# Optimization experiments

Hardware: AMD Instinct MI355X
Metric: run time of the kernel (lower is better)

The kernel has to match this reference:

```python
import jax, jax.numpy as jnp
import numpy as np

B, S, T, E, H, F = 2, 2048, 2048, 1024, 16, 4096
HD = E // H
EPS = 1e-5


def setup_inputs() -> dict:
    key = jax.random.key(0)
    ks = jax.random.split(key, 16)
    def w(k, shape):
        return (jax.random.normal(k, shape, jnp.float32) * 0.02)
    d = {
        "x": jax.random.normal(ks[0], (B, S, E), jnp.float32),
        "enc": jax.random.normal(ks[1], (B, T, E), jnp.float32),
    }
    for i, n in enumerate(["sa_q", "sa_k", "sa_v", "sa_o", "ca_q", "ca_k", "ca_v", "ca_o"]):
        d[n + "w"] = w(ks[2 + i], (E, E))  # torch Linear: [out, in]
        d[n + "b"] = jnp.zeros((E,), jnp.float32)
    d["w1"] = w(ks[10], (F, E)); d["b1"] = jnp.zeros((F,), jnp.float32)
    d["w2"] = w(ks[11], (E, F)); d["b2"] = jnp.zeros((E,), jnp.float32)
    for n in ["ln1", "ln2", "ln3"]:
        d[n + "_g"] = jnp.ones((E,), jnp.float32)
        d[n + "_b"] = jnp.zeros((E,), jnp.float32)
    return d


def _layernorm(x, g, b):
    m = jnp.mean(x, axis=-1, keepdims=True)
    v = jnp.mean((x - m) ** 2, axis=-1, keepdims=True)
    return (x - m) / jnp.sqrt(v + EPS) * g + b


def _heads(x, w, b):
    bsz, sl, _ = x.shape
    y = x @ w.T + b
    return y.reshape(bsz, sl, H, HD).transpose(0, 2, 1, 3)  # [B,H,S,hd]


def _mha(xq, xkv, qw, qb, kw, kb, vw, vb, ow, ob, causal):
    q = _heads(xq, qw, qb)
    k = _heads(xkv, kw, kb)
    v = _heads(xkv, vw, vb)
    scores = jnp.einsum('bhsd,bhtd->bhst', q, k) / np.sqrt(HD).astype(np.float32)
    if causal:
        sl, tl = scores.shape[-2], scores.shape[-1]
        mask = jnp.tril(jnp.ones((sl, tl), bool))
        scores = jnp.where(mask, scores, -jnp.inf)
    a = jax.nn.softmax(scores, axis=-1)
    o = jnp.einsum('bhst,bhtd->bhsd', a, v)
    o = o.transpose(0, 2, 1, 3).reshape(xq.shape[0], xq.shape[1], E)
    return o @ ow.T + ob


def reference(x, enc,
              sa_qw, sa_qb, sa_kw, sa_kb, sa_vw, sa_vb, sa_ow, sa_ob,
              ca_qw, ca_qb, ca_kw, ca_kb, ca_vw, ca_vb, ca_ow, ca_ob,
              w1, b1, w2, b2,
              ln1_g, ln1_b, ln2_g, ln2_b, ln3_g, ln3_b):
    sa = _mha(x, x, sa_qw, sa_qb, sa_kw, sa_kb, sa_vw, sa_vb, sa_ow, sa_ob, True)
    x = _layernorm(x + sa, ln1_g, ln1_b)
    ca = _mha(x, enc, ca_qw, ca_qb, ca_kw, ca_kb, ca_vw, ca_vb, ca_ow, ca_ob, False)
    x = _layernorm(x + ca, ln2_g, ln2_b)
    ffn = jax.nn.relu(x @ w1.T + b1) @ w2.T + b2
    return _layernorm(x + ffn, ln3_g, ln3_b)
```

## Files before the change

kernel.cpp:

```cpp
#include <hip/hip_runtime.h>
#include <hip/hip_bf16.h>
#include <stdint.h>

typedef __attribute__((ext_vector_type(8))) short s16x8;
typedef __attribute__((ext_vector_type(4))) short s16x4;
typedef __attribute__((ext_vector_type(4))) float f32x4;

#define DEV static __device__ __forceinline__

DEV ushort f2bu(float f){
  unsigned u = __builtin_bit_cast(unsigned, f);
  return (ushort)((u + 0x7fffu + ((u >> 16) & 1u)) >> 16);
}
DEV ushort f2bn(float f){
  return __builtin_bit_cast(ushort, __float2bfloat16(f));
}

DEV void gload16(const void* g, void* l){
  __builtin_amdgcn_global_load_lds((const __attribute__((address_space(1))) void*)g,
                                   (__attribute__((address_space(3))) void*)l, 16, 0, 0);
}

struct ConvArgs {
  const float* src[17];
  void*        dst[17];
  int blk_end[17];
  int nel[17];
  unsigned f32mask;
};

__global__ void __launch_bounds__(256) k_conv(ConvArgs a){
  int bi = blockIdx.x, seg = 0;
  while (bi >= a.blk_end[seg]) seg++;
  int b0 = seg ? a.blk_end[seg-1] : 0;
  long off = (long)(bi - b0)*2048 + (long)threadIdx.x*8;
  if (off >= a.nel[seg]) return;
  const float* s = a.src[seg] + off;
  f32x4 v0 = *(const f32x4*)s;
  f32x4 v1 = *(const f32x4*)(s+4);
  if ((a.f32mask >> seg) & 1u){
    float* d = (float*)a.dst[seg] + off;
    *(f32x4*)d = v0; *(f32x4*)(d+4) = v1;
  } else {
    ushort* d = (ushort*)a.dst[seg] + off;
    s16x8 o;
#pragma unroll
    for (int j = 0; j < 4; j++){ o[j] = (short)f2bu(v0[j]); o[4+j] = (short)f2bu(v1[j]); }
    *(s16x8*)d = o;
  }
}

template<int MODE, bool DBUF>
__global__ void __launch_bounds__(256) k_gemm(const ushort* __restrict__ A, const ushort* __restrict__ W,
    const float* __restrict__ bias, float* __restrict__ Cf, ushort* __restrict__ Cb,
    int M, int N, int Kext, int lda, int ldb, long long sstride)
{
  constexpr int NB = DBUF ? 2 : 1;
  __shared__ __align__(16) ushort lsA[NB][128*64];
  __shared__ __align__(16) ushort lsB[NB][128*64];
  const int t = threadIdx.x, w = t >> 6, u = t & 63, lr = u & 15, lk = u >> 4;
  const int m0 = blockIdx.y * 128, n0 = blockIdx.x * 128;
  const int s = blockIdx.z;
  const int wm = w >> 1, wn = w & 1;
  const int rA = t >> 3, c8 = (t & 7) * 8;
  const ushort* Ap = A + (size_t)(m0 + rA) * lda + (size_t)s * Kext + c8;
  const ushort* Wp = W + (size_t)(n0 + rA) * ldb + (size_t)s * Kext + c8;
  if (s){ bias = nullptr; if (Cf) Cf += sstride; }
  f32x4 acc[4][4] = {};
  const int nk = Kext >> 6;

  auto stage = [&](int k0, int buf){
#pragma unroll
    for (int j = 0; j < 4; j++){
      gload16(Ap + (size_t)j*32*lda + k0, &lsA[buf][0] + j*2048 + w*512);
      gload16(Wp + (size_t)j*32*ldb + k0, &lsB[buf][0] + j*2048 + w*512);
    }
  };
  auto body = [&](const ushort* La, const ushort* Lb){
#pragma unroll
    for (int ks = 0; ks < 2; ks++){
      s16x8 af[4], bfr[4];
#pragma unroll
      for (int i = 0; i < 4; i++) af[i]  = *(const s16x8*)(La + (wm*64 + i*16 + lr)*64 + ks*32 + lk*8);
#pragma unroll
      for (int i = 0; i < 4; i++) bfr[i] = *(const s16x8*)(Lb + (wn*64 + i*16 + lr)*64 + ks*32 + lk*8);
#pragma unroll
      for (int mi = 0; mi < 4; mi++)
#pragma unroll
        for (int ni = 0; ni < 4; ni++)
          acc[mi][ni] = __builtin_amdgcn_mfma_f32_16x16x32_bf16(af[mi], bfr[ni], acc[mi][ni], 0, 0, 0);
    }
  };

  if (DBUF){
    stage(0, 0);
    for (int tk = 0; tk < nk; ++tk){
      __syncthreads();
      if (tk + 1 < nk) stage((tk + 1) << 6, (tk + 1) & 1);
      body(&lsA[tk & 1][0], &lsB[tk & 1][0]);
    }
  } else {
    for (int tk = 0; tk < nk; ++tk){
      stage(tk << 6, 0);
      __syncthreads();
      body(&lsA[0][0], &lsB[0][0]);
      __syncthreads();
    }
  }

#pragma unroll
  for (int mi = 0; mi < 4; mi++){
#pragma unroll
    for (int ni = 0; ni < 4; ni++){
      const int row = m0 + wm*64 + mi*16 + lk*4;
      const int col = n0 + wn*64 + ni*16 + lr;
      const float bv = bias ? bias[col] : 0.f;
#pragma unroll
      for (int i = 0; i < 4; i++){
        float v = acc[mi][ni][i] + bv;
        if (MODE == 2) v = fmaxf(v, 0.f);
        size_t idx = (size_t)(row + i) * N + col;
        if (MODE == 1) Cf[idx] = v; else Cb[idx] = f2bn(v);
      }
    }
  }
}

template<int MODE>
__global__ void __launch_bounds__(512, 1) k_gemm256(const ushort* __restrict__ A, const ushort* __restrict__ W,
    const float* __restrict__ bias, float* __restrict__ Cf, ushort* __restrict__ Cb,
    int N, int K, int lda, int ldb)
{
  __shared__ __align__(16) ushort lsA[2][256*64];
  __shared__ __align__(16) ushort lsB[2][256*64];
  const int t = threadIdx.x, w = t >> 6, u = t & 63, lr = u & 15, lk = u >> 4;
  const int gx = gridDim.x;
  const int nwg = gx * gridDim.y;
  const int id = blockIdx.y * gx + blockIdx.x;
  const int swz = (id & 7) * (nwg >> 3) + (id >> 3);
  const int n0 = (swz % gx) * 256, m0 = (swz / gx) * 256;
  const int wm = w >> 2, wn = w & 3;

  const int r0 = w*8 + (u >> 3), cc = u & 7;
  const int csw = 8 * (cc ^ (r0 & 7));
  const ushort* Ap = A + (size_t)(m0 + r0) * lda + csw;
  const ushort* Wp = W + (size_t)(n0 + r0) * ldb + csw;

  f32x4 acc[8][4] = {};
  const int nt = K >> 6;
  const int swl = lr & 7;
  s16x8 afr[4], bfr[4];

#pragma unroll
  for (int j = 0; j < 4; j++){
    gload16(Ap + (size_t)(64*j)*lda, &lsA[0][0] + w*512 + j*4096);
    gload16(Wp + (size_t)(64*j)*ldb, &lsB[0][0] + w*512 + j*4096);
  }
  asm volatile("s_waitcnt vmcnt(0)" ::: "memory");
  __builtin_amdgcn_s_barrier();

  for (int tk = 0; tk < nt; ++tk){
    const char* La = (const char*)&lsA[tk & 1][0];
    const char* Lb = (const char*)&lsB[tk & 1][0];
    ushort* dA = &lsA[(tk & 1) ^ 1][0] + w*512;
    ushort* dB = &lsB[(tk & 1) ^ 1][0] + w*512;
    const bool pf = (tk + 1 < nt);
    const size_t k1 = (size_t)(tk + 1) << 6;

#pragma unroll
    for (int i = 0; i < 4; i++)
      afr[i] = *(const s16x8*)(La + (wm*128 + i*16 + lr)*128 + ((lk ^ swl) * 16));
#pragma unroll
    for (int i = 0; i < 4; i++)
      bfr[i] = *(const s16x8*)(Lb + (wn*64 + i*16 + lr)*128 + ((lk ^ swl) * 16));
    if (pf){
      gload16(Ap + k1, dA);
      gload16(Wp + k1, dB);
      gload16(Ap + (size_t)64*lda + k1, dA + 4096);
      gload16(Wp + (size_t)64*ldb + k1, dB + 4096);
    }
    __builtin_amdgcn_s_barrier();
    asm volatile("s_waitcnt lgkmcnt(0)" ::: "memory");
    __builtin_amdgcn_s_setprio(1);
#pragma unroll
    for (int mi = 0; mi < 4; mi++)
#pragma unroll
      for (int ni = 0; ni < 4; ni++)
        acc[mi][ni] = __builtin_amdgcn_mfma_f32_16x16x32_bf16(afr[mi], bfr[ni], acc[mi][ni], 0, 0, 0);
    __builtin_amdgcn_s_setprio(0);
    __builtin_amdgcn_s_barrier();

#pragma unroll
    for (int i = 0; i < 4; i++)
      afr[i] = *(const s16x8*)(La + (wm*128 + 64 + i*16 + lr)*128 + ((lk ^ swl) * 16));
    if (pf){
      gload16(Ap + (size_t)128*lda + k1, dA + 8192);
      gload16(Wp + (size_t)128*ldb + k1, dB + 8192);
      gload16(Ap + (size_t)192*lda + k1, dA + 12288);
      gload16(Wp + (size_t)192*ldb + k1, dB + 12288);
    }
    __builtin_amdgcn_s_barrier();
    asm volatile("s_waitcnt lgkmcnt(0)" ::: "memory");
    __builtin_amdgcn_s_setprio(1);
#pragma unroll
    for (int mi = 0; mi < 4; mi++)
#pragma unroll
      for (int ni = 0; ni < 4; ni++)
        acc[4+mi][ni] = __builtin_amdgcn_mfma_f32_16x16x32_bf16(afr[mi], bfr[ni], acc[4+mi][ni], 0, 0, 0);
    __builtin_amdgcn_s_setprio(0);
    __builtin_amdgcn_s_barrier();

#pragma unroll
    for (int i = 0; i < 4; i++)
      afr[i] = *(const s16x8*)(La + (wm*128 + i*16 + lr)*128 + (((4 + lk) ^ swl) * 16));
#pragma unroll
    for (int i = 0; i < 4; i++)
      bfr[i] = *(const s16x8*)(Lb + (wn*64 + i*16 + lr)*128 + (((4 + lk) ^ swl) * 16));
    __builtin_amdgcn_s_barrier();
    asm volatile("s_waitcnt lgkmcnt(0)" ::: "memory");
    __builtin_amdgcn_s_setprio(1);
#pragma unroll
    for (int mi = 0; mi < 4; mi++)
#pragma unroll
      for (int ni = 0; ni < 4; ni++)
        acc[mi][ni] = __builtin_amdgcn_mfma_f32_16x16x32_bf16(afr[mi], bfr[ni], acc[mi][ni], 0, 0, 0);
    __builtin_amdgcn_s_setprio(0);
    __builtin_amdgcn_s_barrier();

#pragma unroll
    for (int i = 0; i < 4; i++)
      afr[i] = *(const s16x8*)(La + (wm*128 + 64 + i*16 + lr)*128 + (((4 + lk) ^ swl) * 16));
    __builtin_amdgcn_s_barrier();
    asm volatile("s_waitcnt lgkmcnt(0)" ::: "memory");
    __builtin_amdgcn_s_setprio(1);
#pragma unroll
    for (int mi = 0; mi < 4; mi++)
#pragma unroll
      for (int ni = 0; ni < 4; ni++)
        acc[4+mi][ni] = __builtin_amdgcn_mfma_f32_16x16x32_bf16(afr[mi], bfr[ni], acc[4+mi][ni], 0, 0, 0);
    __builtin_amdgcn_s_setprio(0);
    asm volatile("s_waitcnt vmcnt(0)" ::: "memory");
    __builtin_amdgcn_s_barrier();
  }

#pragma unroll
  for (int mi = 0; mi < 8; mi++){
#pragma unroll
    for (int ni = 0; ni < 4; ni++){
      const int row = m0 + wm*128 + mi*16 + lk*4;
      const int col = n0 + wn*64 + ni*16 + lr;
      const float bv = bias ? bias[col] : 0.f;
#pragma unroll
      for (int i = 0; i < 4; i++){
        float v = acc[mi][ni][i] + bv;
        if (MODE == 2) v = fmaxf(v, 0.f);
        size_t idx = (size_t)(row + i) * N + col;
        if (MODE == 1) Cf[idx] = v; else Cb[idx] = f2bn(v);
      }
    }
  }
}

__global__ void __launch_bounds__(256) k_vt(const ushort* __restrict__ V, ushort* __restrict__ Vt,
                                            int stride, int S)
{
  __shared__ ushort tile[64][72];
  const int st = blockIdx.x*64, h = blockIdx.y, b = blockIdx.z;
  const int r = threadIdx.x >> 3, c8 = (threadIdx.x & 7)*8;
#pragma unroll
  for (int j = 0; j < 2; j++){
    int s = r + j*32;
    s16x8 v = *(const s16x8*)(V + (size_t)(b*S + st + s)*stride + h*64 + c8);
    *(s16x8*)&tile[s][c8] = v;
  }
  __syncthreads();
#pragma unroll
  for (int j = 0; j < 2; j++){
    int d = r + j*32;
    s16x8 o;
#pragma unroll
    for (int e = 0; e < 8; e++) o[e] = tile[c8+e][d];
    *(s16x8*)(Vt + ((size_t)((b*16 + h)*64 + d))*S + st + c8) = o;
  }
}

template<bool CAUSAL>
__global__ void __launch_bounds__(512) k_attn(const ushort* __restrict__ Q, const ushort* __restrict__ Kg,
    const ushort* __restrict__ Vt, ushort* __restrict__ O, int sQ, int sK, int SQ, int SKV)
{
  __shared__ __align__(16) ushort Kl[2][64*64];
  __shared__ __align__(16) ushort Vl[2][64*64];
  __shared__ __align__(16) ushort Pl[8][16*64];
  const int t = threadIdx.x, w = t >> 6, u = t & 63, lr = u & 15, lk = u >> 4;
  const int hb = blockIdx.x;
  const int b = hb >> 4, h = hb & 15;
  const int srow = t >> 3, scol = t & 7;
  const size_t kvbase = (size_t)b * SKV;
  const size_t vtbase = (size_t)((b*16 + h)*64);
  char* Pc = (char*)&Pl[w][0];
  const int swzq = (lr & 7) << 4;
  const float c = 0.18033688f;

  auto stage = [&](int kt, int buf){
    gload16(Kg + (kvbase + kt*64 + srow)*sK + h*64 + 8*(scol ^ (srow & 7)), &Kl[buf][0] + w*512);
    gload16(Vt + (vtbase + srow)*SKV + kt*64 + 8*(scol ^ (srow & 7)), &Vl[buf][0] + w*512);
  };

  const int NREP = CAUSAL ? 2 : 1;
#pragma unroll 1
  for (int rep = 0; rep < NREP; rep++){
    const int qt = CAUSAL ? (rep ? blockIdx.y : 2*gridDim.y - 1 - blockIdx.y) : blockIdx.y;
    const int q0 = qt * 128;

    const ushort* qp = Q + (size_t)(b*SQ + q0 + w*16 + lr) * sQ + h*64 + lk*8;
    s16x8 qf0 = *(const s16x8*)qp;
    s16x8 qf1 = *(const s16x8*)(qp + 32);

    f32x4 oacc[4] = {};
    f32x4 lacc = {};
    const int nkt = CAUSAL ? (2*qt + 2) : (SKV >> 6);

    stage(0, 0);
    __syncthreads();

    for (int kt = 0; kt < nkt; kt++){
      const int buf = kt & 1;
      if (kt + 1 < nkt) stage(kt + 1, buf ^ 1);
      char* Kc = (char*)&Kl[buf][0];
      char* Vc = (char*)&Vl[buf][0];

      f32x4 sacc[4] = {};
#pragma unroll
      for (int ks = 0; ks < 2; ks++){
        s16x8 qf = ks ? qf1 : qf0;
#pragma unroll
        for (int ni = 0; ni < 4; ni++){
          int key = ni*16 + lr;
          s16x8 kf = *(const s16x8*)(Kc + key*128 + ((ks*64 + lk*16) ^ ((key & 7) << 4)));
          sacc[ni] = __builtin_amdgcn_mfma_f32_16x16x32_bf16(kf, qf, sacc[ni], 0, 0, 0);
        }
      }
      if (CAUSAL && kt >= 2*qt){
        const int koff = kt*64 - q0;
#pragma unroll
        for (int ni = 0; ni < 4; ni++)
#pragma unroll
          for (int i = 0; i < 4; i++)
            if (koff + 16*ni + lk*4 + i > w*16 + lr) sacc[ni][i] = -1e30f;
      }

#pragma unroll
      for (int ni = 0; ni < 4; ni++){
#pragma unroll
        for (int i = 0; i < 4; i++) sacc[ni][i] = __builtin_exp2f(sacc[ni][i] * c);
        lacc += sacc[ni];
      }

#pragma unroll
      for (int ni = 0; ni < 4; ni++){
        s16x4 pk;
#pragma unroll
        for (int i = 0; i < 4; i++) pk[i] = (short)f2bn(sacc[ni][i]);
        *(s16x4*)(Pc + lr*128 + ((32*ni + 8*lk) ^ swzq)) = pk;
      }

#pragma unroll
      for (int ks = 0; ks < 2; ks++){
        s16x8 pf = *(const s16x8*)(Pc + lr*128 + ((ks*64 + lk*16) ^ swzq));
#pragma unroll
        for (int ni = 0; ni < 4; ni++){
          int d = ni*16 + lr;
          s16x8 vf = *(const s16x8*)(Vc + d*128 + ((ks*64 + lk*16) ^ ((d & 7) << 4)));
          oacc[ni] = __builtin_amdgcn_mfma_f32_16x16x32_bf16(pf, vf, oacc[ni], 0, 0, 0);
        }
      }
      __syncthreads();
    }

    float lrun = lacc[0] + lacc[1] + lacc[2] + lacc[3];
    lrun += __shfl_xor(lrun, 16);
    lrun += __shfl_xor(lrun, 32);
    float il = 1.f / lrun;
    float invl[4];
#pragma unroll
    for (int i = 0; i < 4; i++) invl[i] = __shfl(il, lk*4 + i);
#pragma unroll
    for (int ni = 0; ni < 4; ni++)
#pragma unroll
      for (int i = 0; i < 4; i++)
        O[(size_t)(b*SQ + q0 + w*16 + lk*4 + i)*1024 + h*64 + ni*16 + lr] = f2bn(oacc[ni][i] * invl[i]);
  }
}

template<bool WB16>
__global__ void __launch_bounds__(256) k_ln(const float* __restrict__ R, const float* __restrict__ P,
    const float* __restrict__ P2, const float* __restrict__ G, const float* __restrict__ Bv,
    float* __restrict__ Of, ushort* __restrict__ Ob)
{
  const int row = blockIdx.x, t = threadIdx.x, w = t >> 6, u = t & 63;
  const size_t base = (size_t)row * 1024 + t * 4;
  f32x4 r = *(const f32x4*)(R + base);
  f32x4 p = *(const f32x4*)(P + base);
  f32x4 v = r + p;
  if (P2){ f32x4 p2 = *(const f32x4*)(P2 + base); v += p2; }
  float s = 0.f, q = 0.f;
#pragma unroll
  for (int j = 0; j < 4; j++){ s += v[j]; q += v[j]*v[j]; }
#pragma unroll
  for (int md = 1; md < 64; md <<= 1){ s += __shfl_xor(s, md); q += __shfl_xor(q, md); }
  __shared__ float ps[4], pq[4];
  if (u == 0){ ps[w] = s; pq[w] = q; }
  __syncthreads();
  s = ps[0] + ps[1] + ps[2] + ps[3];
  q = pq[0] + pq[1] + pq[2] + pq[3];
  const float mean = s * (1.f/1024.f);
  const float var  = q * (1.f/1024.f) - mean*mean;
  const float rstd = rsqrtf(var + 1e-5f);
  f32x4 g4 = *(const f32x4*)(G  + t*4);
  f32x4 b4 = *(const f32x4*)(Bv + t*4);
  f32x4 o;
#pragma unroll
  for (int j = 0; j < 4; j++) o[j] = (v[j] - mean) * rstd * g4[j] + b4[j];
  *(f32x4*)(Of + base) = o;
  if (WB16){
    s16x4 ob;
#pragma unroll
    for (int j = 0; j < 4; j++) ob[j] = (short)f2bn(o[j]);
    *(s16x4*)(Ob + base) = ob;
  }
}

extern "C" void kernel_launch(void* const* d_in, const int* in_sizes, int n_in,
                              void* d_out, int out_size, void* d_ws, size_t ws_size,
                              hipStream_t stream)
{
  const float* x   = (const float*)d_in[0];
  const float* enc = (const float*)d_in[1];
  const float* aw[8]; const float* ab[8];
  for (int i = 0; i < 8; i++){ aw[i] = (const float*)d_in[2 + 2*i]; ab[i] = (const float*)d_in[3 + 2*i]; }
  const float* w1 = (const float*)d_in[18]; const float* b1 = (const float*)d_in[19];
  const float* w2 = (const float*)d_in[20]; const float* b2 = (const float*)d_in[21];
  const float* lg[3] = {(const float*)d_in[22], (const float*)d_in[24], (const float*)d_in[26]};
  const float* lb[3] = {(const float*)d_in[23], (const float*)d_in[25], (const float*)d_in[27]};
  float* out = (float*)d_out;

  const size_t MB = 1024ull * 1024ull;
  if (ws_size < 129 * MB) return;
  char* ws = (char*)d_ws;
  ushort* wqkv = (ushort*)(ws + 0*MB);
  ushort* wcq  = (ushort*)(ws + 6*MB);
  ushort* wkv  = (ushort*)(ws + 8*MB);
  ushort* wo1w = (ushort*)(ws + 12*MB);
  ushort* wo2w = (ushort*)(ws + 14*MB);
  ushort* w1b  = (ushort*)(ws + 16*MB);
  ushort* w2b  = (ushort*)(ws + 24*MB);
  ushort* xb   = (ushort*)(ws + 32*MB);
  ushort* encb = (ushort*)(ws + 40*MB);
  ushort* attb = (ushort*)(ws + 48*MB);
  float*  proj = (float*)(ws + 56*MB);
  float*  x1f  = (float*)(ws + 72*MB);
  ushort* xab  = (ushort*)(ws + 88*MB);
  ushort* QKVb    = (ushort*)(ws + 96*MB);
  ushort* Vt1     = (ushort*)(ws + 120*MB);
  ushort* crossQb = (ushort*)(ws + 96*MB);
  ushort* encKVb  = (ushort*)(ws + 104*MB);
  ushort* Vt2     = (ushort*)(ws + 120*MB);
  ushort* hb      = (ushort*)(ws + 96*MB);
  float*  proj2wo  = (float*)(ws + 96*MB);
  float*  proj2ffn = (float*)(ws + 32*MB);
  float*  bqkv = (float*)(ws + 128*MB);
  float*  bkv  = (float*)(ws + 128*MB + 16384);

  const long long ssWO  = ((long long)(96 - 56) * (long long)MB) / 4;
  const long long ssFFN = ((long long)(32 - 56) * (long long)MB) / 4;

  ConvArgs ca;
  const float* srcs[17] = { x, enc, aw[0], aw[1], aw[2], aw[3], aw[4], aw[5], aw[6], aw[7],
                            w1, w2, ab[0], ab[1], ab[2], ab[5], ab[6] };
  void* dsts[17] = { xb, encb, wqkv, wqkv + 1048576, wqkv + 2097152, wo1w, wcq, wkv, wkv + 1048576, wo2w,
                     w1b, w2b, bqkv, bqkv + 1024, bqkv + 2048, bkv, bkv + 1024 };
  int nels[17] = { 4194304, 4194304, 1048576, 1048576, 1048576, 1048576, 1048576, 1048576, 1048576, 1048576,
                   4194304, 4194304, 1024, 1024, 1024, 1024, 1024 };
  int acc_blk = 0;
  for (int i = 0; i < 17; i++){
    ca.src[i] = srcs[i]; ca.dst[i] = dsts[i]; ca.nel[i] = nels[i];
    acc_blk += (nels[i] + 2047) / 2048;
    ca.blk_end[i] = acc_blk;
  }
  ca.f32mask = 0x1F000u;
  k_conv<<<acc_blk, 256, 0, stream>>>(ca);

  auto gemm = [&](const ushort* A, const ushort* W, const float* bias, float* Cf, ushort* Cb,
                  int M, int N, int Kext, int lda, int ldb, int mode, bool dbuf,
                  int nsplit, long long sstride){
    dim3 g(N/128, M/128, nsplit);
    if (dbuf){
      if (mode == 0)      k_gemm<0,true ><<<g, 256, 0, stream>>>(A, W, bias, Cf, Cb, M, N, Kext, lda, ldb, sstride);
      else if (mode == 1) k_gemm<1,true ><<<g, 256, 0, stream>>>(A, W, bias, Cf, Cb, M, N, Kext, lda, ldb, sstride);
      else                k_gemm<2,true ><<<g, 256, 0, stream>>>(A, W, bias, Cf, Cb, M, N, Kext, lda, ldb, sstride);
    } else {
      if (mode == 0)      k_gemm<0,false><<<g, 256, 0, stream>>>(A, W, bias, Cf, Cb, M, N, Kext, lda, ldb, sstride);
      else if (mode == 1) k_gemm<1,false><<<g, 256, 0, stream>>>(A, W, bias, Cf, Cb, M, N, Kext, lda, ldb, sstride);
      else                k_gemm<2,false><<<g, 256, 0, stream>>>(A, W, bias, Cf, Cb, M, N, Kext, lda, ldb, sstride);
    }
  };

  k_gemm256<0><<<dim3(12,16), 512, 0, stream>>>(xb, wqkv, bqkv, nullptr, QKVb, 3072, 1024, 1024, 1024);
  k_vt<<<dim3(32,16,2), 256, 0, stream>>>(QKVb + 2048, Vt1, 3072, 2048);
  k_attn<true><<<dim3(32,8), 512, 0, stream>>>(QKVb, QKVb + 1024, Vt1, attb, 3072, 3072, 2048, 2048);
  gemm(attb, wo1w, ab[3], proj, nullptr, 4096, 1024, 512, 1024, 1024, 1, true, 2, ssWO);
  k_ln<true><<<4096, 256, 0, stream>>>(x, proj, proj2wo, lg[0], lb[0], x1f, xab);

  gemm(xab,  wcq, ab[4], nullptr, crossQb, 4096, 1024, 1024, 1024, 1024, 0, true, 1, 0);
  k_gemm256<0><<<dim3(8,16), 512, 0, stream>>>(encb, wkv, bkv, nullptr, encKVb, 2048, 1024, 1024, 1024);
  k_vt<<<dim3(32,16,2), 256, 0, stream>>>(encKVb + 1024, Vt2, 2048, 2048);
  k_attn<false><<<dim3(32,16), 512, 0, stream>>>(crossQb, encKVb, Vt2, attb, 1024, 2048, 2048, 2048);
  gemm(attb, wo2w, ab[7], proj, nullptr, 4096, 1024, 512, 1024, 1024, 1, true, 2, ssWO);
  k_ln<true><<<4096, 256, 0, stream>>>(x1f, proj, proj2wo, lg[1], lb[1], x1f, xab);

  k_gemm256<2><<<dim3(16,16), 512, 0, stream>>>(xab, w1b, b1, nullptr, hb, 4096, 1024, 1024, 1024);
  gemm(hb,  w2b, b2, proj, nullptr, 4096, 1024, 2048, 4096, 4096, 1, true, 2, ssFFN);
  k_ln<false><<<4096, 256, 0, stream>>>(x1f, proj, proj2ffn, lg[2], lb[2], out, nullptr);
}
```

Measured before the change: 408.3 us.

## Split attention along the key dimension into two halves and add a combine kernel

```diff
diff --git a/kernel.cpp b/kernel.cpp
--- a/kernel.cpp
+++ b/kernel.cpp
@@ -15,6 +15,7 @@
 DEV ushort f2bn(float f){
   return __builtin_bit_cast(ushort, __float2bfloat16(f));
 }
+DEV float b2f(short v){ return __builtin_bit_cast(float, ((unsigned)(ushort)v) << 16); }
 
 DEV void gload16(const void* g, void* l){
   __builtin_amdgcn_global_load_lds((const __attribute__((address_space(1))) void*)g,
@@ -286,7 +287,8 @@
 
 template<bool CAUSAL>
 __global__ void __launch_bounds__(512) k_attn(const ushort* __restrict__ Q, const ushort* __restrict__ Kg,
-    const ushort* __restrict__ Vt, ushort* __restrict__ O, int sQ, int sK, int SQ, int SKV)
+    const ushort* __restrict__ Vt, ushort* __restrict__ O, ushort* __restrict__ OpP, float* __restrict__ LpP,
+    int sQ, int sK, int SQ, int SKV)
 {
   __shared__ __align__(16) ushort Kl[2][64*64];
   __shared__ __align__(16) ushort Vl[2][64*64];
@@ -294,6 +296,7 @@
   const int t = threadIdx.x, w = t >> 6, u = t & 63, lr = u & 15, lk = u >> 4;
   const int hb = blockIdx.x;
   const int b = hb >> 4, h = hb & 15;
+  const int s = blockIdx.z;
   const int srow = t >> 3, scol = t & 7;
   const size_t kvbase = (size_t)b * SKV;
   const size_t vtbase = (size_t)((b*16 + h)*64);
@@ -306,30 +309,26 @@
     gload16(Vt + (vtbase + srow)*SKV + kt*64 + 8*(scol ^ (srow & 7)), &Vl[buf][0] + w*512);
   };
 
-  const int NREP = CAUSAL ? 2 : 1;
-#pragma unroll 1
-  for (int rep = 0; rep < NREP; rep++){
-    const int qt = CAUSAL ? (rep ? blockIdx.y : 2*gridDim.y - 1 - blockIdx.y) : blockIdx.y;
+  auto process = [&](int qt, int kt0, int kt1, ushort* op, float* lp){
     const int q0 = qt * 128;
-
     const ushort* qp = Q + (size_t)(b*SQ + q0 + w*16 + lr) * sQ + h*64 + lk*8;
     s16x8 qf0 = *(const s16x8*)qp;
     s16x8 qf1 = *(const s16x8*)(qp + 32);
 
     f32x4 oacc[4] = {};
     f32x4 lacc = {};
-    const int nkt = CAUSAL ? (2*qt + 2) : (SKV >> 6);
-
-    stage(0, 0);
+
+    stage(kt0, kt0 & 1);
     __syncthreads();
 
-    for (int kt = 0; kt < nkt; kt++){
+    for (int kt = kt0; kt < kt1; kt++){
       const int buf = kt & 1;
-      if (kt + 1 < nkt) stage(kt + 1, buf ^ 1);
+      if (kt + 1 < kt1) stage(kt + 1, buf ^ 1);
       char* Kc = (char*)&Kl[buf][0];
       char* Vc = (char*)&Vl[buf][0];
 
       f32x4 sacc[4] = {};
+      __builtin_amdgcn_s_setprio(1);
 #pragma unroll
       for (int ks = 0; ks < 2; ks++){
         s16x8 qf = ks ? qf1 : qf0;
@@ -340,6 +339,7 @@
           sacc[ni] = __builtin_amdgcn_mfma_f32_16x16x32_bf16(kf, qf, sacc[ni], 0, 0, 0);
         }
       }
+      __builtin_amdgcn_s_setprio(0);
       if (CAUSAL && kt >= 2*qt){
         const int koff = kt*64 - q0;
 #pragma unroll
@@ -364,6 +364,7 @@
         *(s16x4*)(Pc + lr*128 + ((32*ni + 8*lk) ^ swzq)) = pk;
       }
 
+      __builtin_amdgcn_s_setprio(1);
 #pragma unroll
       for (int ks = 0; ks < 2; ks++){
         s16x8 pf = *(const s16x8*)(Pc + lr*128 + ((ks*64 + lk*16) ^ swzq));
@@ -374,22 +375,77 @@
           oacc[ni] = __builtin_amdgcn_mfma_f32_16x16x32_bf16(pf, vf, oacc[ni], 0, 0, 0);
         }
       }
+      __builtin_amdgcn_s_setprio(0);
       __syncthreads();
     }
 
     float lrun = lacc[0] + lacc[1] + lacc[2] + lacc[3];
     lrun += __shfl_xor(lrun, 16);
     lrun += __shfl_xor(lrun, 32);
-    float il = 1.f / lrun;
-    float invl[4];
-#pragma unroll
-    for (int i = 0; i < 4; i++) invl[i] = __shfl(il, lk*4 + i);
-#pragma unroll
-    for (int ni = 0; ni < 4; ni++)
-#pragma unroll
-      for (int i = 0; i < 4; i++)
-        O[(size_t)(b*SQ + q0 + w*16 + lk*4 + i)*1024 + h*64 + ni*16 + lr] = f2bn(oacc[ni][i] * invl[i]);
-  }
+
+    if (lp){
+      if (lk == 0) lp[w*16 + lr] = lrun;
+#pragma unroll
+      for (int ni = 0; ni < 4; ni++)
+#pragma unroll
+        for (int i = 0; i < 4; i++)
+          op[(size_t)(w*16 + lk*4 + i)*64 + ni*16 + lr] = f2bn(oacc[ni][i]);
+    } else {
+      float il = 1.f / lrun;
+      float invl[4];
+#pragma unroll
+      for (int i = 0; i < 4; i++) invl[i] = __shfl(il, lk*4 + i);
+#pragma unroll
+      for (int ni = 0; ni < 4; ni++)
+#pragma unroll
+        for (int i = 0; i < 4; i++)
+          O[(size_t)(b*SQ + q0 + w*16 + lk*4 + i)*1024 + h*64 + ni*16 + lr] = f2bn(oacc[ni][i] * invl[i]);
+    }
+  };
+
+  if (CAUSAL){
+    const int y = blockIdx.y;
+    const int qtA = 15 - y, qtB = y;
+    const int nktA = 2*qtA + 2;
+    const long pb = (long)(((s*2 + b)*16 + h)*8 + y);
+    ushort* op = OpP + pb * (128*64);
+    float*  lp = LpP + pb * 128;
+    if (s == 0){
+      process(qtA, 0, 17, op, lp);
+    } else {
+      process(qtA, 17, nktA, op, lp);
+      process(qtB, 0, 2*qtB + 2, nullptr, nullptr);
+    }
+  } else {
+    const int qt = blockIdx.y;
+    const long pb = (long)(((s*2 + b)*16 + h)*2048 + qt*128);
+    process(qt, s*16, s*16 + 16, OpP + pb*64, LpP + pb);
+  }
+}
+
+template<int MODE>
+__global__ void __launch_bounds__(256) k_comb(const ushort* __restrict__ Op, const float* __restrict__ Lp,
+                                              ushort* __restrict__ Oo)
+{
+  const int idx = blockIdx.x*32 + (threadIdx.x >> 3);
+  const int d0 = (threadIdx.x & 7)*8;
+  const int SR = MODE ? 65536 : 32768;
+  const float l = Lp[idx] + Lp[idx + SR];
+  s16x8 a = *(const s16x8*)(Op + (size_t)idx*64 + d0);
+  s16x8 cB = *(const s16x8*)(Op + (size_t)(idx + SR)*64 + d0);
+  const float il = 1.f / l;
+  s16x8 o;
+#pragma unroll
+  for (int j = 0; j < 8; j++) o[j] = (short)f2bn((b2f(a[j]) + b2f(cB[j])) * il);
+  int q, h, bb;
+  if (MODE){
+    q = idx & 2047; h = (idx >> 11) & 15; bb = idx >> 15;
+  } else {
+    int row = idx & 127, y = (idx >> 7) & 7;
+    h = (idx >> 10) & 15; bb = idx >> 14;
+    q = (15 - y)*128 + row;
+  }
+  *(s16x8*)(Oo + ((size_t)(bb*2048 + q))*1024 + h*64 + d0) = o;
 }
 
 template<bool WB16>
@@ -468,6 +524,10 @@
   ushort* hb      = (ushort*)(ws + 96*MB);
   float*  proj2wo  = (float*)(ws + 96*MB);
   float*  proj2ffn = (float*)(ws + 32*MB);
+  ushort* OpA = (ushort*)(ws + 56*MB);
+  float*  LpA = (float*)(ws + 66*MB);
+  ushort* OpX = (ushort*)(ws + 32*MB);
+  float*  LpX = (float*)(ws + 56*MB);
   float*  bqkv = (float*)(ws + 128*MB);
   float*  bkv  = (float*)(ws + 128*MB + 16384);
 
@@ -507,14 +567,16 @@
 
   k_gemm256<0><<<dim3(12,16), 512, 0, stream>>>(xb, wqkv, bqkv, nullptr, QKVb, 3072, 1024, 1024, 1024);
   k_vt<<<dim3(32,16,2), 256, 0, stream>>>(QKVb + 2048, Vt1, 3072, 2048);
-  k_attn<true><<<dim3(32,8), 512, 0, stream>>>(QKVb, QKVb + 1024, Vt1, attb, 3072, 3072, 2048, 2048);
+  k_attn<true><<<dim3(32,8,2), 512, 0, stream>>>(QKVb, QKVb + 1024, Vt1, attb, OpA, LpA, 3072, 3072, 2048, 2048);
+  k_comb<0><<<1024, 256, 0, stream>>>(OpA, LpA, attb);
   gemm(attb, wo1w, ab[3], proj, nullptr, 4096, 1024, 512, 1024, 1024, 1, true, 2, ssWO);
   k_ln<true><<<4096, 256, 0, stream>>>(x, proj, proj2wo, lg[0], lb[0], x1f, xab);
 
   gemm(xab,  wcq, ab[4], nullptr, crossQb, 4096, 1024, 1024, 1024, 1024, 0, true, 1, 0);
   k_gemm256<0><<<dim3(8,16), 512, 0, stream>>>(encb, wkv, bkv, nullptr, encKVb, 2048, 1024, 1024, 1024);
   k_vt<<<dim3(32,16,2), 256, 0, stream>>>(encKVb + 1024, Vt2, 2048, 2048);
-  k_attn<false><<<dim3(32,16), 512, 0, stream>>>(crossQb, encKVb, Vt2, attb, 1024, 2048, 2048, 2048);
+  k_attn<false><<<dim3(32,16,2), 512, 0, stream>>>(crossQb, encKVb, Vt2, attb, OpX, LpX, 1024, 2048, 2048, 2048);
+  k_comb<1><<<2048, 256, 0, stream>>>(OpX, LpX, attb);
   gemm(attb, wo2w, ab[7], proj, nullptr, 4096, 1024, 512, 1024, 1024, 1, true, 2, ssWO);
   k_ln<true><<<4096, 256, 0, stream>>>(x1f, proj, proj2wo, lg[1], lb[1], x1f, xab);
 
```

Result: no change. 405.0 us (-0.8%).

## Use 256-tile split-K GEMM for projections and fold softmax scale into Q

Applied to the files above, without the earlier changes.

```diff
diff --git a/kernel.cpp b/kernel.cpp
--- a/kernel.cpp
+++ b/kernel.cpp
@@ -20,6 +20,8 @@
   __builtin_amdgcn_global_load_lds((const __attribute__((address_space(1))) void*)g,
                                    (__attribute__((address_space(3))) void*)l, 16, 0, 0);
 }
+
+#define SCALE_C 0.18033688f
 
 struct ConvArgs {
   const float* src[17];
@@ -50,24 +52,20 @@
   }
 }
 
-template<int MODE, bool DBUF>
 __global__ void __launch_bounds__(256) k_gemm(const ushort* __restrict__ A, const ushort* __restrict__ W,
-    const float* __restrict__ bias, float* __restrict__ Cf, ushort* __restrict__ Cb,
-    int M, int N, int Kext, int lda, int ldb, long long sstride)
+    const float* __restrict__ bias, ushort* __restrict__ Cb,
+    int M, int N, int K, int lda, int ldb, float scale)
 {
-  constexpr int NB = DBUF ? 2 : 1;
-  __shared__ __align__(16) ushort lsA[NB][128*64];
-  __shared__ __align__(16) ushort lsB[NB][128*64];
+  __shared__ __align__(16) ushort lsA[2][128*64];
+  __shared__ __align__(16) ushort lsB[2][128*64];
   const int t = threadIdx.x, w = t >> 6, u = t & 63, lr = u & 15, lk = u >> 4;
   const int m0 = blockIdx.y * 128, n0 = blockIdx.x * 128;
-  const int s = blockIdx.z;
   const int wm = w >> 1, wn = w & 1;
   const int rA = t >> 3, c8 = (t & 7) * 8;
-  const ushort* Ap = A + (size_t)(m0 + rA) * lda + (size_t)s * Kext + c8;
-  const ushort* Wp = W + (size_t)(n0 + rA) * ldb + (size_t)s * Kext + c8;
-  if (s){ bias = nullptr; if (Cf) Cf += sstride; }
+  const ushort* Ap = A + (size_t)(m0 + rA) * lda + c8;
+  const ushort* Wp = W + (size_t)(n0 + rA) * ldb + c8;
   f32x4 acc[4][4] = {};
-  const int nk = Kext >> 6;
+  const int nk = K >> 6;
 
   auto stage = [&](int k0, int buf){
 #pragma unroll
@@ -76,7 +74,12 @@
       gload16(Wp + (size_t)j*32*ldb + k0, &lsB[buf][0] + j*2048 + w*512);
     }
   };
-  auto body = [&](const ushort* La, const ushort* Lb){
+  stage(0, 0);
+  for (int tk = 0; tk < nk; ++tk){
+    __syncthreads();
+    if (tk + 1 < nk) stage((tk + 1) << 6, (tk + 1) & 1);
+    const ushort* La = &lsA[tk & 1][0];
+    const ushort* Lb = &lsB[tk & 1][0];
 #pragma unroll
     for (int ks = 0; ks < 2; ks++){
       s16x8 af[4], bfr[4];
@@ -89,22 +92,6 @@
 #pragma unroll
         for (int ni = 0; ni < 4; ni++)
           acc[mi][ni] = __builtin_amdgcn_mfma_f32_16x16x32_bf16(af[mi], bfr[ni], acc[mi][ni], 0, 0, 0);
-    }
-  };
-
-  if (DBUF){
-    stage(0, 0);
-    for (int tk = 0; tk < nk; ++tk){
-      __syncthreads();
-      if (tk + 1 < nk) stage((tk + 1) << 6, (tk + 1) & 1);
-      body(&lsA[tk & 1][0], &lsB[tk & 1][0]);
-    }
-  } else {
-    for (int tk = 0; tk < nk; ++tk){
-      stage(tk << 6, 0);
-      __syncthreads();
-      body(&lsA[0][0], &lsB[0][0]);
-      __syncthreads();
     }
   }
 
@@ -114,22 +101,22 @@
     for (int ni = 0; ni < 4; ni++){
       const int row = m0 + wm*64 + mi*16 + lk*4;
       const int col = n0 + wn*64 + ni*16 + lr;
-      const float bv = bias ? bias[col] : 0.f;
+      const float bv = bias[col];
 #pragma unroll
       for (int i = 0; i < 4; i++){
-        float v = acc[mi][ni][i] + bv;
-        if (MODE == 2) v = fmaxf(v, 0.f);
-        size_t idx = (size_t)(row + i) * N + col;
-        if (MODE == 1) Cf[idx] = v; else Cb[idx] = f2bn(v);
-      }
-    }
-  }
-}
+        float v = (acc[mi][ni][i] + bv) * scale;
+        Cb[(size_t)(row + i) * N + col] = f2bn(v);
+      }
+    }
+  }
+}
+
+struct CfP { float* p[3]; };
 
 template<int MODE>
 __global__ void __launch_bounds__(512, 1) k_gemm256(const ushort* __restrict__ A, const ushort* __restrict__ W,
-    const float* __restrict__ bias, float* __restrict__ Cf, ushort* __restrict__ Cb,
-    int N, int K, int lda, int ldb)
+    const float* __restrict__ bias, CfP cf, ushort* __restrict__ Cb,
+    int N, int Ktot, int lda, int ldb, int scaleLim, float scale)
 {
   __shared__ __align__(16) ushort lsA[2][256*64];
   __shared__ __align__(16) ushort lsB[2][256*64];
@@ -140,14 +127,17 @@
   const int swz = (id & 7) * (nwg >> 3) + (id >> 3);
   const int n0 = (swz % gx) * 256, m0 = (swz / gx) * 256;
   const int wm = w >> 2, wn = w & 3;
+  const int s = blockIdx.z, NS = gridDim.z;
+  const int ntT = Ktot >> 6;
+  const int kb = (s * ntT) / NS;
+  const int nt = ((s + 1) * ntT) / NS - kb;
 
   const int r0 = w*8 + (u >> 3), cc = u & 7;
   const int csw = 8 * (cc ^ (r0 & 7));
-  const ushort* Ap = A + (size_t)(m0 + r0) * lda + csw;
-  const ushort* Wp = W + (size_t)(n0 + r0) * ldb + csw;
+  const ushort* Ap = A + (size_t)(m0 + r0) * lda + csw + (size_t)kb * 64;
+  const ushort* Wp = W + (size_t)(n0 + r0) * ldb + csw + (size_t)kb * 64;
 
   f32x4 acc[8][4] = {};
-  const int nt = K >> 6;
   const int swl = lr & 7;
   s16x8 afr[4], bfr[4];
 
@@ -243,17 +233,19 @@
     __builtin_amdgcn_s_barrier();
   }
 
+  float* Cf = (MODE == 1) ? cf.p[s] : nullptr;
 #pragma unroll
   for (int mi = 0; mi < 8; mi++){
 #pragma unroll
     for (int ni = 0; ni < 4; ni++){
       const int row = m0 + wm*128 + mi*16 + lk*4;
       const int col = n0 + wn*64 + ni*16 + lr;
-      const float bv = bias ? bias[col] : 0.f;
+      const float bv = (s == 0) ? bias[col] : 0.f;
 #pragma unroll
       for (int i = 0; i < 4; i++){
         float v = acc[mi][ni][i] + bv;
         if (MODE == 2) v = fmaxf(v, 0.f);
+        if (MODE == 0 && col < scaleLim) v *= scale;
         size_t idx = (size_t)(row + i) * N + col;
         if (MODE == 1) Cf[idx] = v; else Cb[idx] = f2bn(v);
       }
@@ -299,7 +291,6 @@
   const size_t vtbase = (size_t)((b*16 + h)*64);
   char* Pc = (char*)&Pl[w][0];
   const int swzq = (lr & 7) << 4;
-  const float c = 0.18033688f;
 
   auto stage = [&](int kt, int buf){
     gload16(Kg + (kvbase + kt*64 + srow)*sK + h*64 + 8*(scol ^ (srow & 7)), &Kl[buf][0] + w*512);
@@ -309,7 +300,8 @@
   const int NREP = CAUSAL ? 2 : 1;
 #pragma unroll 1
   for (int rep = 0; rep < NREP; rep++){
-    const int qt = CAUSAL ? (rep ? blockIdx.y : 2*gridDim.y - 1 - blockIdx.y) : blockIdx.y;
+    const int qt = CAUSAL ? (rep ? (int)blockIdx.y : (int)(2*gridDim.y - 1 - blockIdx.y))
+                          : (int)blockIdx.y;
     const int q0 = qt * 128;
 
     const ushort* qp = Q + (size_t)(b*SQ + q0 + w*16 + lr) * sQ + h*64 + lk*8;
@@ -330,6 +322,7 @@
       char* Vc = (char*)&Vl[buf][0];
 
       f32x4 sacc[4] = {};
+      __builtin_amdgcn_s_setprio(1);
 #pragma unroll
       for (int ks = 0; ks < 2; ks++){
         s16x8 qf = ks ? qf1 : qf0;
@@ -340,6 +333,7 @@
           sacc[ni] = __builtin_amdgcn_mfma_f32_16x16x32_bf16(kf, qf, sacc[ni], 0, 0, 0);
         }
       }
+      __builtin_amdgcn_s_setprio(0);
       if (CAUSAL && kt >= 2*qt){
         const int koff = kt*64 - q0;
 #pragma unroll
@@ -352,7 +346,7 @@
 #pragma unroll
       for (int ni = 0; ni < 4; ni++){
 #pragma unroll
-        for (int i = 0; i < 4; i++) sacc[ni][i] = __builtin_exp2f(sacc[ni][i] * c);
+        for (int i = 0; i < 4; i++) sacc[ni][i] = __builtin_exp2f(sacc[ni][i]);
         lacc += sacc[ni];
       }
 
@@ -364,6 +358,7 @@
         *(s16x4*)(Pc + lr*128 + ((32*ni + 8*lk) ^ swzq)) = pk;
       }
 
+      __builtin_amdgcn_s_setprio(1);
 #pragma unroll
       for (int ks = 0; ks < 2; ks++){
         s16x8 pf = *(const s16x8*)(Pc + lr*128 + ((ks*64 + lk*16) ^ swzq));
@@ -374,6 +369,7 @@
           oacc[ni] = __builtin_amdgcn_mfma_f32_16x16x32_bf16(pf, vf, oacc[ni], 0, 0, 0);
         }
       }
+      __builtin_amdgcn_s_setprio(0);
       __syncthreads();
     }
 
@@ -394,7 +390,8 @@
 
 template<bool WB16>
 __global__ void __launch_bounds__(256) k_ln(const float* __restrict__ R, const float* __restrict__ P,
-    const float* __restrict__ P2, const float* __restrict__ G, const float* __restrict__ Bv,
+    const float* __restrict__ P2, const float* __restrict__ P3,
+    const float* __restrict__ G, const float* __restrict__ Bv,
     float* __restrict__ Of, ushort* __restrict__ Ob)
 {
   const int row = blockIdx.x, t = threadIdx.x, w = t >> 6, u = t & 63;
@@ -403,6 +400,7 @@
   f32x4 p = *(const f32x4*)(P + base);
   f32x4 v = r + p;
   if (P2){ f32x4 p2 = *(const f32x4*)(P2 + base); v += p2; }
+  if (P3){ f32x4 p3 = *(const f32x4*)(P3 + base); v += p3; }
   float s = 0.f, q = 0.f;
 #pragma unroll
   for (int j = 0; j < 4; j++){ s += v[j]; q += v[j]*v[j]; }
@@ -466,13 +464,11 @@
   ushort* encKVb  = (ushort*)(ws + 104*MB);
   ushort* Vt2     = (ushort*)(ws + 120*MB);
   ushort* hb      = (ushort*)(ws + 96*MB);
-  float*  proj2wo  = (float*)(ws + 96*MB);
-  float*  proj2ffn = (float*)(ws + 32*MB);
+  float*  pWO     = (float*)(ws + 96*MB);
+  float*  pF1     = (float*)(ws + 0*MB);
+  float*  pF2     = (float*)(ws + 32*MB);
   float*  bqkv = (float*)(ws + 128*MB);
   float*  bkv  = (float*)(ws + 128*MB + 16384);
-
-  const long long ssWO  = ((long long)(96 - 56) * (long long)MB) / 4;
-  const long long ssFFN = ((long long)(32 - 56) * (long long)MB) / 4;
 
   ConvArgs ca;
   const float* srcs[17] = { x, enc, aw[0], aw[1], aw[2], aw[3], aw[4], aw[5], aw[6], aw[7],
@@ -490,35 +486,25 @@
   ca.f32mask = 0x1F000u;
   k_conv<<<acc_blk, 256, 0, stream>>>(ca);
 
-  auto gemm = [&](const ushort* A, const ushort* W, const float* bias, float* Cf, ushort* Cb,
-                  int M, int N, int Kext, int lda, int ldb, int mode, bool dbuf,
-                  int nsplit, long long sstride){
-    dim3 g(N/128, M/128, nsplit);
-    if (dbuf){
-      if (mode == 0)      k_gemm<0,true ><<<g, 256, 0, stream>>>(A, W, bias, Cf, Cb, M, N, Kext, lda, ldb, sstride);
-      else if (mode == 1) k_gemm<1,true ><<<g, 256, 0, stream>>>(A, W, bias, Cf, Cb, M, N, Kext, lda, ldb, sstride);
-      else                k_gemm<2,true ><<<g, 256, 0, stream>>>(A, W, bias, Cf, Cb, M, N, Kext, lda, ldb, sstride);
-    } else {
-      if (mode == 0)      k_gemm<0,false><<<g, 256, 0, stream>>>(A, W, bias, Cf, Cb, M, N, Kext, lda, ldb, sstride);
-      else if (mode == 1) k_gemm<1,false><<<g, 256, 0, stream>>>(A, W, bias, Cf, Cb, M, N, Kext, lda, ldb, sstride);
-      else                k_gemm<2,false><<<g, 256, 0, stream>>>(A, W, bias, Cf, Cb, M, N, Kext, lda, ldb, sstride);
-    }
-  };
-
-  k_gemm256<0><<<dim3(12,16), 512, 0, stream>>>(xb, wqkv, bqkv, nullptr, QKVb, 3072, 1024, 1024, 1024);
+  CfP none = {};
+
+  k_gemm256<0><<<dim3(12,16,1), 512, 0, stream>>>(xb, wqkv, bqkv, none, QKVb, 3072, 1024, 1024, 1024, 1024, SCALE_C);
   k_vt<<<dim3(32,16,2), 256, 0, stream>>>(QKVb + 2048, Vt1, 3072, 2048);
   k_attn<true><<<dim3(32,8), 512, 0, stream>>>(QKVb, QKVb + 1024, Vt1, attb, 3072, 3072, 2048, 2048);
-  gemm(attb, wo1w, ab[3], proj, nullptr, 4096, 1024, 512, 1024, 1024, 1, true, 2, ssWO);
-  k_ln<true><<<4096, 256, 0, stream>>>(x, proj, proj2wo, lg[0], lb[0], x1f, xab);
-
-  gemm(xab,  wcq, ab[4], nullptr, crossQb, 4096, 1024, 1024, 1024, 1024, 0, true, 1, 0);
-  k_gemm256<0><<<dim3(8,16), 512, 0, stream>>>(encb, wkv, bkv, nullptr, encKVb, 2048, 1024, 1024, 1024);
+  { CfP cp = { { proj, pWO, nullptr } };
+    k_gemm256<1><<<dim3(4,16,2), 512, 0, stream>>>(attb, wo1w, ab[3], cp, nullptr, 1024, 1024, 1024, 1024, 0, 1.f); }
+  k_ln<true><<<4096, 256, 0, stream>>>(x, proj, pWO, nullptr, lg[0], lb[0], x1f, xab);
+
+  k_gemm<<<dim3(8,32), 256, 0, stream>>>(xab, wcq, ab[4], crossQb, 4096, 1024, 1024, 1024, 1024, SCALE_C);
+  k_gemm256<0><<<dim3(8,16,1), 512, 0, stream>>>(encb, wkv, bkv, none, encKVb, 2048, 1024, 1024, 1024, 0, 1.f);
   k_vt<<<dim3(32,16,2), 256, 0, stream>>>(encKVb + 1024, Vt2, 2048, 2048);
   k_attn<false><<<dim3(32,16), 512, 0, stream>>>(crossQb, encKVb, Vt2, attb, 1024, 2048, 2048, 2048);
-  gemm(attb, wo2w, ab[7], proj, nullptr, 4096, 1024, 512, 1024, 1024, 1, true, 2, ssWO);
-  k_ln<true><<<4096, 256, 0, stream>>>(x1f, proj, proj2wo, lg[1], lb[1], x1f, xab);
-
-  k_gemm256<2><<<dim3(16,16), 512, 0, stream>>>(xab, w1b, b1, nullptr, hb, 4096, 1024, 1024, 1024);
-  gemm(hb,  w2b, b2, proj, nullptr, 4096, 1024, 2048, 4096, 4096, 1, true, 2, ssFFN);
-  k_ln<false><<<4096, 256, 0, stream>>>(x1f, proj, proj2ffn, lg[2], lb[2], out, nullptr);
-}
+  { CfP cp = { { proj, pWO, nullptr } };
+    k_gemm256<1><<<dim3(4,16,2), 512, 0, stream>>>(attb, wo2w, ab[7], cp, nullptr, 1024, 1024, 1024, 1024, 0, 1.f); }
+  k_ln<true><<<4096, 256, 0, stream>>>(x1f, proj, pWO, nullptr, lg[1], lb[1], x1f, xab);
+
+  k_gemm256<2><<<dim3(16,16,1), 512, 0, stream>>>(xab, w1b, b1, none, hb, 4096, 1024, 1024, 1024, 0, 1.f);
+  { CfP cp = { { proj, pF1, pF2 } };
+    k_gemm256<1><<<dim3(4,16,3), 512, 0, stream>>>(hb, w2b, b2, cp, nullptr, 1024, 4096, 4096, 4096, 0, 1.f); }
+  k_ln<false><<<4096, 256, 0, stream>>>(x1f, proj, pF1, pF2, lg[2], lb[2], out, nullptr);
+}
```

New measurement: 413.7 us. No clear change (+1.3%).
